# Performance work log

Measured on AMD Instinct MI355X. Metric: run time of the kernel, lower is better.

## Reference

```python
import math
import jax, jax.numpy as jnp
import numpy as np

H = 16          # num attention heads
D = 64          # head dim
BUCKETS = 256   # position_buckets
MAX_POS = 512   # max_relative_positions
ATT_SPAN = BUCKETS  # pos_ebd_size A
SCALE_FACTOR = 3    # 1 + len(['c2p','p2c'])


def _log_bucket(rel):
    # log-bucketed relative positions (DeBERTa-v2 _make_log_bucket_position)
    mid = BUCKETS // 2
    rel = jnp.clip(rel, -MAX_POS + 1, MAX_POS - 1)
    sign = jnp.sign(rel).astype(jnp.float32)
    abs_pos = jnp.maximum(jnp.abs(rel), 1)
    log_base = math.log((MAX_POS - 1) / mid)
    log_pos = jnp.ceil(jnp.log(abs_pos.astype(jnp.float32) / mid) / log_base * (mid - 1)) + mid
    bucket = jnp.where(abs_pos < mid, abs_pos.astype(jnp.float32), log_pos) * sign
    return bucket.astype(jnp.int32)


def _rel_pos(q_len, k_len):
    q = jnp.arange(q_len, dtype=jnp.int32)
    k = jnp.arange(k_len, dtype=jnp.int32)
    return _log_bucket(q[:, None] - k[None, :])  # (Q, K)


def setup_inputs() -> dict:
    key = jax.random.key(0)
    ks = jax.random.split(key, 6)
    B, S, Hd = 4, 1024, 1024
    std = 0.02
    return {
        "hidden_states": jax.random.normal(ks[0], (B, S, Hd), jnp.float32),
        "rel_embeddings": jax.random.normal(ks[1], (2 * ATT_SPAN, Hd), jnp.float32) * std,
        "Wq": jax.random.normal(ks[2], (Hd, H * D), jnp.float32) * std,
        "bq": jnp.zeros((H * D,), jnp.float32),
        "Wk": jax.random.normal(ks[3], (Hd, H * D), jnp.float32) * std,
        "bk": jnp.zeros((H * D,), jnp.float32),
        "Wv": jax.random.normal(ks[4], (Hd, H * D), jnp.float32) * std,
        "bv": jnp.zeros((H * D,), jnp.float32),
    }


def reference(hidden_states, rel_embeddings, Wq, bq, Wk, bk, Wv, bv):
    B, S, Hd = hidden_states.shape
    A2 = 2 * ATT_SPAN

    def heads(x):  # (B,S,H*D) -> (B,H,S,D)
        return x.reshape(B, S, H, D).transpose(0, 2, 1, 3)

    q = heads(hidden_states @ Wq + bq)
    k = heads(hidden_states @ Wk + bk)
    v = heads(hidden_states @ Wv + bv)

    scale = math.sqrt(D * SCALE_FACTOR)
    scores = jnp.einsum('bhqd,bhkd->bhqk', q, k) / scale  # (B,H,S,S)

    rel = _rel_pos(S, S)  # (S,S) int32 bucketed relative ids
    # share_att_key=True: pos key/query use key_proj/query_proj
    pos_k = (rel_embeddings @ Wk + bk).reshape(A2, H, D).transpose(1, 0, 2)  # (H,2A,D)
    pos_q = (rel_embeddings @ Wq + bq).reshape(A2, H, D).transpose(1, 0, 2)  # (H,2A,D)

    # c2p: content->position
    c2p = jnp.einsum('bhqd,hkd->bhqk', q, pos_k)  # (B,H,S,2A)
    c2p_idx = jnp.clip(rel + ATT_SPAN, 0, A2 - 1)  # (S,S)
    c2p = jnp.take_along_axis(c2p, jnp.broadcast_to(c2p_idx[None, None], (B, H, S, S)), axis=-1) / scale

    # p2c: position->content
    p2c = jnp.einsum('bhkd,hqd->bhkq', k, pos_q)  # (B,H,S,2A)
    p2c_idx = jnp.clip(-rel + ATT_SPAN, 0, A2 - 1)  # (S,S)
    p2c = jnp.take_along_axis(p2c, jnp.broadcast_to(p2c_idx[None, None], (B, H, S, S)), axis=-1)
    p2c = jnp.swapaxes(p2c, -1, -2) / scale

    probs = jax.nn.softmax(scores + c2p + p2c, axis=-1)
    ctx = jnp.einsum('bhqk,bhkd->bhqd', probs, v)  # (B,H,S,D)
    return ctx.transpose(0, 2, 1, 3).reshape(B, S, H * D)
```

## Files before the change

### kernel.cpp

```cpp
#include <hip/hip_runtime.h>
#include <hip/hip_bf16.h>
#include <math.h>

typedef __attribute__((ext_vector_type(8))) short v8s;
typedef __attribute__((ext_vector_type(4))) short v4sh;
typedef __attribute__((ext_vector_type(4))) unsigned short v4us;
typedef __attribute__((ext_vector_type(4))) float v4f;
typedef __attribute__((ext_vector_type(4))) int   v4i;

#define AS1(p) ((const __attribute__((address_space(1))) void*)(p))
#define AS3(p) ((__attribute__((address_space(3))) void*)(p))

__device__ inline unsigned short f2b(float f){
  __hip_bfloat16 h = __float2bfloat16(f);
  return __builtin_bit_cast(unsigned short, h);
}
__device__ inline float b2f(unsigned short u){
  __hip_bfloat16 h = __builtin_bit_cast(__hip_bfloat16, u);
  return __bfloat162float(h);
}
__device__ inline unsigned cvtpk(float lo, float hi){
  unsigned d;
  asm("v_cvt_pk_bf16_f32 %0, %1, %2" : "=v"(d) : "v"(lo), "v"(hi));
  return d;
}

__device__ inline int bucket_id(int i){
  int r = i - 1023;
  if (r > 511) r = 511; if (r < -511) r = -511;
  float sign = (r > 0) ? 1.f : ((r < 0) ? -1.f : 0.f);
  int ap = r < 0 ? -r : r; if (ap < 1) ap = 1;
  float bucket;
  if (ap < 128) bucket = (float)ap * sign;
  else {
    float lp = ceilf(logf((float)ap / 128.f) / logf(511.f/128.f) * 127.f) + 128.f;
    bucket = lp * sign;
  }
  int idx = (int)bucket + 256;
  if (idx < 0) idx = 0; if (idx > 511) idx = 511;
  return idx;
}

__global__ __launch_bounds__(256) void pack_x(const float* __restrict__ hs,
                                              const float* __restrict__ rel,
                                              const float* __restrict__ Wq,
                                              const float* __restrict__ Wk,
                                              const float* __restrict__ Wv,
                                              unsigned short* __restrict__ X,
                                              unsigned short* __restrict__ Wt3,
                                              short* __restrict__ tab,
                                              unsigned long long* __restrict__ tab64){
  __shared__ unsigned short t[64][65];
  int blk = blockIdx.x;
  if (blk < 2304){
    const int HT8 = 4096*1024/8;
    int i8 = blk*256 + threadIdx.x;
    const float* src = (i8 < HT8) ? (hs + (size_t)i8*8) : (rel + ((size_t)i8 - HT8)*8);
    v8s o;
    #pragma unroll
    for (int j = 0; j < 8; j++) o[j] = (short)f2b(src[j]);
    *(v8s*)&X[(size_t)i8*8] = o;
    return;
  }
  if (blk < 2313){
    int i = (blk - 2304)*256 + threadIdx.x;
    if (i < 2047) tab[i] = (short)bucket_id(i);
    if (i < 2056){
      unsigned long long w = 0;
      #pragma unroll
      for (int r = 0; r < 4; r++)
        w |= (unsigned long long)(unsigned short)bucket_id(i + r) << (16*r);
      tab64[i] = w;
    }
    return;
  }
  int tb = blk - 2313;
  int wsel = tb >> 8, bx = tb & 255;
  const float* in = (wsel == 0) ? Wq : ((wsel == 1) ? Wk : Wv);
  unsigned short* outp = Wt3 + ((size_t)wsel << 20);
  int r0 = (bx >> 4) << 6, c0 = (bx & 15) << 6;
  int tx = threadIdx.x & 63, ty = threadIdx.x >> 6;
  #pragma unroll
  for (int p = 0; p < 16; p++){ int r = (p<<2)+ty; t[tx][r] = f2b(in[(size_t)(r0+r)*1024 + c0+tx]); }
  __syncthreads();
  #pragma unroll
  for (int p = 0; p < 16; p++){ int c = (p<<2)+ty; outp[(size_t)(c0+c)*1024 + r0+tx] = t[c][tx]; }
}

__global__ __launch_bounds__(256) void gemm_qkv(
    const unsigned short* __restrict__ A,
    const unsigned short* __restrict__ Bt3,
    unsigned short* __restrict__ Qa, unsigned short* __restrict__ Ka,
    unsigned short* __restrict__ VtT,
    const float* __restrict__ bq, const float* __restrict__ bk,
    const float* __restrict__ bv, float alpha_q)
{
  __shared__ unsigned short smem[2*128*64];
  unsigned short* a_tile = smem;
  unsigned short* b_tile = smem + 128*64;
  int nb = (blockIdx.x & 7)*108 + (blockIdx.x >> 3);
  int bm = nb / 24, bn = nb % 24;
  int m0 = bm << 7, n0 = bn << 7;
  int tid = threadIdx.x, lane = tid & 63, wave = tid >> 6;
  int l15 = lane & 15, lhi = lane >> 4;
  int rbase = (wave >> 1) << 6, cbase = (wave & 1) << 6;
  int crow[4], csw[4];
  #pragma unroll
  for (int u = 0; u < 4; u++){
    int ch = tid + (u << 8);
    crow[u] = ch >> 3;
    csw[u] = ((ch & 7) ^ (crow[u] & 7)) << 3;
  }
  v4f acc[4][4] = {};
  for (int kt = 0; kt < 1024; kt += 64){
    #pragma unroll
    for (int u = 0; u < 4; u++){
      int ch = tid + (u << 8);
      __builtin_amdgcn_global_load_lds(AS1(A   + (size_t)(m0 + crow[u])*1024 + kt + csw[u]),
                                       AS3(a_tile + (size_t)ch*8), 16, 0, 0);
      __builtin_amdgcn_global_load_lds(AS1(Bt3 + (size_t)(n0 + crow[u])*1024 + kt + csw[u]),
                                       AS3(b_tile + (size_t)ch*8), 16, 0, 0);
    }
    __syncthreads();
    #pragma unroll
    for (int ks = 0; ks < 2; ks++){
      v8s af[4], bfr[4];
      int kb = (ks << 2) + lhi;
      #pragma unroll
      for (int i = 0; i < 4; i++){
        int r = rbase + (i << 4) + l15;
        af[i] = *(const v8s*)&a_tile[r*64 + ((kb ^ (r & 7)) << 3)];
      }
      #pragma unroll
      for (int j = 0; j < 4; j++){
        int r = cbase + (j << 4) + l15;
        bfr[j] = *(const v8s*)&b_tile[r*64 + ((kb ^ (r & 7)) << 3)];
      }
      #pragma unroll
      for (int i = 0; i < 4; i++)
        #pragma unroll
        for (int j = 0; j < 4; j++)
          acc[i][j] = __builtin_amdgcn_mfma_f32_16x16x32_bf16(af[i], bfr[j], acc[i][j], 0, 0, 0);
    }
    __syncthreads();
  }
  int seg = n0 >> 10;
  int nn0 = n0 & 1023;
  if (seg == 2){
    if (m0 >= 4096) return;
    int bb = m0 >> 10, s0 = m0 & 1023;
    #pragma unroll
    for (int i = 0; i < 4; i++){
      int r = rbase + (i << 4) + (lhi << 2);
      #pragma unroll
      for (int j = 0; j < 4; j++){
        int c = cbase + (j << 4) + l15;
        float bvv = bv[nn0 + c];
        #pragma unroll
        for (int rr = 0; rr < 4; rr++)
          smem[c*128 + ((r + rr) ^ ((c & 7) << 4))] = f2b(acc[i][j][rr] + bvv);
      }
    }
    __syncthreads();
    int v = tid >> 3, sc = (tid & 7) << 4;
    #pragma unroll
    for (int vb = 0; vb < 4; vb++){
      int vv = v + (vb << 5);
      #pragma unroll
      for (int c2 = 0; c2 < 2; c2++){
        int sb = sc + (c2 << 3);
        v8s val = *(const v8s*)&smem[vv*128 + (sb ^ ((vv & 7) << 4))];
        *(v8s*)&VtT[((size_t)(bb << 10) + nn0 + vv)*1024 + s0 + sb] = val;
      }
    }
    return;
  }
  unsigned short* C = (seg == 0) ? Qa : Ka;
  const float* bias = (seg == 0) ? bq : bk;
  float alpha = (seg == 0) ? alpha_q : 1.f;
  #pragma unroll
  for (int i = 0; i < 4; i++){
    int row = rbase + (i << 4) + (lhi << 2);
    #pragma unroll
    for (int j = 0; j < 4; j++){
      int col = cbase + (j << 4) + l15;
      float bvv = bias[nn0 + col];
      #pragma unroll
      for (int r = 0; r < 4; r++)
        smem[(row + r)*128 + (col ^ (((row + r) & 7) << 4))] = f2b((acc[i][j][r] + bvv) * alpha);
    }
  }
  __syncthreads();
  #pragma unroll
  for (int c = 0; c < 8; c++){
    int row = (tid >> 4) + (c << 4);
    int col8 = (tid & 15) << 3;
    v8s val = *(const v8s*)&smem[row*128 + (col8 ^ ((row & 7) << 4))];
    *(v8s*)&C[(size_t)(m0 + row)*1024 + nn0 + col8] = val;
  }
}

__global__ __launch_bounds__(256) void gemm_pos(
    const unsigned short* __restrict__ Qa,
    const unsigned short* __restrict__ Ka,
    unsigned short* __restrict__ C2P,
    unsigned short* __restrict__ P2C)
{
  __shared__ unsigned short smem[2*128*64];
  unsigned short* a_tile = smem;
  unsigned short* b_tile = smem + 128*64;
  int tab = blockIdx.y >> 4, h = blockIdx.y & 15;
  int bm = blockIdx.x >> 2, bn = blockIdx.x & 3;
  int m0 = bm << 7, n0 = bn << 7;
  const unsigned short* A  = tab ? Ka : Qa;
  const unsigned short* Bt = tab ? Qa : Ka;
  unsigned short* C = tab ? P2C : C2P;
  int tid = threadIdx.x, lane = tid & 63, wave = tid >> 6;
  int l15 = lane & 15, lhi = lane >> 4;
  int rbase = (wave >> 1) << 6, cbase = (wave & 1) << 6;
  #pragma unroll
  for (int u = 0; u < 4; u++){
    int ch = tid + (u << 8);
    int row = ch >> 3;
    int csw = ((ch & 7) ^ (row & 7)) << 3;
    __builtin_amdgcn_global_load_lds(AS1(A  + (size_t)(m0 + row)*1024 + (h << 6) + csw),
                                     AS3(a_tile + (size_t)ch*8), 16, 0, 0);
    __builtin_amdgcn_global_load_lds(AS1(Bt + (size_t)(4096 + n0 + row)*1024 + (h << 6) + csw),
                                     AS3(b_tile + (size_t)ch*8), 16, 0, 0);
  }
  __syncthreads();
  v4f acc[4][4] = {};
  #pragma unroll
  for (int ks = 0; ks < 2; ks++){
    v8s af[4], bfr[4];
    int kb = (ks << 2) + lhi;
    #pragma unroll
    for (int i = 0; i < 4; i++){
      int r = rbase + (i << 4) + l15;
      af[i] = *(const v8s*)&a_tile[r*64 + ((kb ^ (r & 7)) << 3)];
    }
    #pragma unroll
    for (int j = 0; j < 4; j++){
      int r = cbase + (j << 4) + l15;
      bfr[j] = *(const v8s*)&b_tile[r*64 + ((kb ^ (r & 7)) << 3)];
    }
    #pragma unroll
    for (int i = 0; i < 4; i++)
      #pragma unroll
      for (int j = 0; j < 4; j++)
        acc[i][j] = __builtin_amdgcn_mfma_f32_16x16x32_bf16(af[i], bfr[j], acc[i][j], 0, 0, 0);
  }
  __syncthreads();
  #pragma unroll
  for (int i = 0; i < 4; i++){
    int row = rbase + (i << 4) + (lhi << 2);
    #pragma unroll
    for (int j = 0; j < 4; j++){
      int col = cbase + (j << 4) + l15;
      #pragma unroll
      for (int r = 0; r < 4; r++)
        smem[(row + r)*128 + (col ^ (((row + r) & 7) << 4))] = f2b(acc[i][j][r]);
    }
  }
  __syncthreads();
  #pragma unroll
  for (int c = 0; c < 8; c++){
    int row = (tid >> 4) + (c << 4);
    int col8 = (tid & 15) << 3;
    v8s val = *(const v8s*)&smem[row*128 + (col8 ^ ((row & 7) << 4))];
    *(v8s*)&C[(size_t)(m0 + row)*8192 + (h << 9) + n0 + col8] = val;
  }
}

__global__ __launch_bounds__(256) void attn(
  const unsigned short* __restrict__ Qall,
  const unsigned short* __restrict__ Kall,
  const unsigned short* __restrict__ Vt,
  const unsigned short* __restrict__ c2p,
  const unsigned short* __restrict__ p2c,
  const short* __restrict__ idxt,
  const unsigned long long* __restrict__ t64g,
  float* __restrict__ out)
{
  __shared__ unsigned short k_lds[64*64];
  __shared__ unsigned short v_lds[64*64];
  __shared__ unsigned short cw[64*72];
  __shared__ unsigned short pw[64*72];
  __shared__ short basc[16*64];
  __shared__ short basp[16*64];

  int bid = blockIdx.x;
  int xcd = bid & 7, jj = bid >> 3;
  int bh = (xcd << 3) + (jj >> 4), qb = jj & 15;
  int b = bh >> 4, h = bh & 15;
  int q0 = qb << 6;
  int tid = threadIdx.x, lane = tid & 63, wave = tid >> 6;
  int l15 = lane & 15, lhi = lane >> 4;

  #pragma unroll
  for (int v = 0; v < 8; v++){
    int i = tid + (v << 8);
    int kt = (i >> 6) & 15, row = i & 63;
    if (i < 1024){
      int bc = idxt[q0 + row - (kt << 6) + 960] & ~7;
      basc[(kt << 6) + row] = (short)(row*72 - bc);
    } else {
      int bp = idxt[q0 + 1023 - (kt << 6) - row] & ~7;
      basp[(kt << 6) + row] = (short)(row*72 - bp);
    }
  }

  int qrow = q0 + (wave << 4) + l15;
  v8s aq[2];
  #pragma unroll
  for (int ks = 0; ks < 2; ks++)
    aq[ks] = *(const v8s*)&Qall[(size_t)((b << 10) + qrow)*1024 + (h << 6) + (ks << 5) + (lhi << 3)];

  int prow_[3], pcc_[3]; bool pval[3];
  #pragma unroll
  for (int u = 0; u < 3; u++){
    int pp = tid + (u << 8);
    pval[u] = pp < 576;
    prow_[u] = pp / 9; pcc_[u] = pp - prow_[u]*9;
  }
  const size_t cbase0 = ((size_t)((b << 10) + q0))*8192 + (h << 9);
  const size_t pbase0 = ((size_t)(b << 10))*8192 + (h << 9);

  unsigned long long t64u[4];

  auto issue_kwin = [&](int kt){
    int k0 = kt << 6;
    #pragma unroll
    for (int u = 0; u < 2; u++){
      int ch = tid + (u << 8);
      int rr = ch >> 3, seg = ch & 7;
      int csw = (seg ^ (rr & 7)) << 3;
      __builtin_amdgcn_global_load_lds(AS1(Kall + (size_t)((b << 10) + k0 + rr)*1024 + (h << 6) + csw),
                                       AS3(k_lds + (size_t)ch*8), 16, 0, 0);
    }
    #pragma unroll
    for (int u = 0; u < 3; u++){
      if (pval[u]){
        int row = prow_[u], cc = pcc_[u];
        int bc = row*72 - (int)basc[(kt << 6) + row];
        __builtin_amdgcn_global_load_lds(AS1(c2p + cbase0 + (size_t)row*8192 + bc + (cc << 3)),
                                         AS3(cw + (size_t)(tid + (u << 8))*8), 16, 0, 0);
      int bp = row*72 - (int)basp[(kt << 6) + row];
        __builtin_amdgcn_global_load_lds(AS1(p2c + pbase0 + (size_t)(k0 + row)*8192 + bp + (cc << 3)),
                                         AS3(pw + (size_t)(tid + (u << 8))*8), 16, 0, 0);
      }
    }
  };
  auto issue_tv = [&](int kt){
    int k0 = kt << 6;
    int Bc = q0 - k0 + (wave << 4) + l15 - (lhi << 2) + 1020;
    #pragma unroll
    for (int j = 0; j < 4; j++) t64u[j] = t64g[Bc - (j << 4)];
    __builtin_amdgcn_sched_barrier(0);
    #pragma unroll
    for (int u = 0; u < 2; u++){
      int ch = tid + (u << 8);
      int rr = ch >> 3, seg = ch & 7;
      int csw = (seg ^ (rr & 7)) << 3;
      __builtin_amdgcn_global_load_lds(AS1(Vt + (size_t)((b << 10) + (h << 6) + rr)*1024 + k0 + csw),
                                       AS3(v_lds + (size_t)ch*8), 16, 0, 0);
    }
  };

  v4f o_acc[4] = {};
  float m_run = -INFINITY, l_part = 0.f;

  __syncthreads();
  issue_kwin(0);
  __builtin_amdgcn_sched_barrier(0);
  issue_tv(0);

  for (int kt = 0; kt < 16; kt++){
    asm volatile("s_waitcnt vmcnt(6)" ::: "memory");
    __builtin_amdgcn_sched_barrier(0);
    __builtin_amdgcn_s_barrier();
    __builtin_amdgcn_sched_barrier(0);

    v4f s_acc[4] = {};
    #pragma unroll
    for (int j = 0; j < 4; j++){
      int krow = (j << 4) + l15;
      #pragma unroll
      for (int ks = 0; ks < 2; ks++){
        v8s kf = *(const v8s*)&k_lds[krow*64 + ((((ks << 2) + lhi) ^ (krow & 7)) << 3)];
        s_acc[j] = __builtin_amdgcn_mfma_f32_16x16x32_bf16(kf, aq[ks], s_acc[j], 0, 0, 0);
      }
    }
    int cvq = (int)basc[(kt << 6) + (wave << 4) + l15];
    #pragma unroll
    for (int j = 0; j < 4; j++){
      v4sh bp4 = *(const v4sh*)&basp[(kt << 6) + (j << 4) + (lhi << 2)];
      v4us idv = __builtin_bit_cast(v4us, t64u[j]);
      #pragma unroll
      for (int r = 0; r < 4; r++){
        int id = (int)idv[3 - r];
        s_acc[j][r] += b2f(cw[cvq + id]) + b2f(pw[(int)bp4[r] + id]);
      }
    }
    float lmax = s_acc[0][0];
    #pragma unroll
    for (int j = 0; j < 4; j++)
      #pragma unroll
      for (int r = 0; r < 4; r++) lmax = fmaxf(lmax, s_acc[j][r]);
    if (__any(lmax > m_run + 6.f)){
      float mx = lmax;
      mx = fmaxf(mx, __shfl_xor(mx, 16));
      mx = fmaxf(mx, __shfl_xor(mx, 32));
      float mnew = fmaxf(m_run, mx);
      float corr = exp2f(m_run - mnew);
      m_run = mnew;
      l_part *= corr;
      float co[4];
      #pragma unroll
      for (int r = 0; r < 4; r++) co[r] = __shfl(corr, (lhi << 2) + r);
      #pragma unroll
      for (int j = 0; j < 4; j++)
        #pragma unroll
        for (int r = 0; r < 4; r++) o_acc[j][r] *= co[r];
    }
    unsigned wj[4][2];
    float ps = 0.f;
    #pragma unroll
    for (int j = 0; j < 4; j++){
      float p0 = exp2f(s_acc[j][0] - m_run);
      float p1 = exp2f(s_acc[j][1] - m_run);
      float p2 = exp2f(s_acc[j][2] - m_run);
      float p3 = exp2f(s_acc[j][3] - m_run);
      ps += (p0 + p1) + (p2 + p3);
      wj[j][0] = cvtpk(p0, p1);
      wj[j][1] = cvtpk(p2, p3);
    }
    l_part += ps;
    #pragma unroll
    for (int p = 0; p < 2; p++){
      asm("v_permlane32_swap_b32 %0, %1" : "+v"(wj[0][p]), "+v"(wj[1][p]));
      asm("v_permlane32_swap_b32 %0, %1" : "+v"(wj[2][p]), "+v"(wj[3][p]));
      asm("v_permlane16_swap_b32 %0, %1" : "+v"(wj[0][p]), "+v"(wj[1][p]));
      asm("v_permlane16_swap_b32 %0, %1" : "+v"(wj[2][p]), "+v"(wj[3][p]));
    }
    v4i pai0 = { (int)wj[0][0], (int)wj[0][1], (int)wj[1][0], (int)wj[1][1] };
    v4i pai1 = { (int)wj[2][0], (int)wj[2][1], (int)wj[3][0], (int)wj[3][1] };
    v8s pa0 = __builtin_bit_cast(v8s, pai0);
    v8s pa1 = __builtin_bit_cast(v8s, pai1);

    asm volatile("s_waitcnt vmcnt(0)" ::: "memory");
    __builtin_amdgcn_sched_barrier(0);
    __builtin_amdgcn_s_barrier();
    __builtin_amdgcn_sched_barrier(0);

    if (kt < 15) issue_kwin(kt + 1);
    __builtin_amdgcn_sched_barrier(0);

    #pragma unroll
    for (int j = 0; j < 4; j++){
      int vrow = (j << 4) + l15;
      v8s vb0 = *(const v8s*)&v_lds[vrow*64 + (((lhi) ^ (vrow & 7)) << 3)];
      o_acc[j] = __builtin_amdgcn_mfma_f32_16x16x32_bf16(pa0, vb0, o_acc[j], 0, 0, 0);
      v8s vb1 = *(const v8s*)&v_lds[vrow*64 + (((4 + lhi) ^ (vrow & 7)) << 3)];
      o_acc[j] = __builtin_amdgcn_mfma_f32_16x16x32_bf16(pa1, vb1, o_acc[j], 0, 0, 0);
    }
    if (kt < 15){
      asm volatile("s_waitcnt lgkmcnt(0)" ::: "memory");
      __builtin_amdgcn_sched_barrier(0);
      __builtin_amdgcn_s_barrier();
      __builtin_amdgcn_sched_barrier(0);
      issue_tv(kt + 1);
    }
  }
  float ls = l_part;
  ls += __shfl_xor(ls, 16);
  ls += __shfl_xor(ls, 32);
  float inv = 1.f / ls;
  float io[4];
  #pragma unroll
  for (int r = 0; r < 4; r++) io[r] = __shfl(inv, (lhi << 2) + r);
  #pragma unroll
  for (int r = 0; r < 4; r++){
    int row = q0 + (wave << 4) + (lhi << 2) + r;
    #pragma unroll
    for (int j = 0; j < 4; j++)
      out[(size_t)((b << 10) + row)*1024 + (h << 6) + (j << 4) + l15] = o_acc[j][r] * io[r];
  }
}

extern "C" void kernel_launch(void* const* d_in, const int* in_sizes, int n_in,
                              void* d_out, int out_size, void* d_ws, size_t ws_size,
                              hipStream_t stream)
{
  const float* hs  = (const float*)d_in[0];
  const float* rel = (const float*)d_in[1];
  const float* Wq  = (const float*)d_in[2];
  const float* bq  = (const float*)d_in[3];
  const float* Wk  = (const float*)d_in[4];
  const float* bk  = (const float*)d_in[5];
  const float* Wv  = (const float*)d_in[6];
  const float* bv  = (const float*)d_in[7];
  float* out = (float*)d_out;

  char* ws = (char*)d_ws;
  size_t off = 0;
  auto alloc = [&](size_t bytes) -> void* {
    void* p = ws + off; off += (bytes + 255) & ~(size_t)255; return p;
  };
  short*              idxt  = (short*)             alloc(2047 * 2);
  unsigned long long* tab64 = (unsigned long long*)alloc(2056 * 8);
  unsigned short* Xb   = (unsigned short*)alloc((size_t)4608*1024*2);
  unsigned short* Wt3  = (unsigned short*)alloc((size_t)3072*1024*2);
  unsigned short* Qa   = (unsigned short*)alloc((size_t)4608*1024*2);
  unsigned short* Ka   = (unsigned short*)alloc((size_t)4608*1024*2);
  unsigned short* VtT  = (unsigned short*)alloc((size_t)4096*1024*2);
  unsigned short* C2P  = (unsigned short*)alloc((size_t)4096*8192*2);
  unsigned short* P2C  = (unsigned short*)alloc((size_t)4096*8192*2);
  (void)                                  alloc(4096);
  (void)ws_size; (void)in_sizes; (void)n_in; (void)out_size;

  pack_x<<<3081, 256, 0, stream>>>(hs, rel, Wq, Wk, Wv, Xb, Wt3, idxt, tab64);

  const float alpha_q = 1.4426950408889634f / sqrtf(192.f);
  gemm_qkv<<<864, 256, 0, stream>>>(Xb, Wt3, Qa, Ka, VtT, bq, bk, bv, alpha_q);

  gemm_pos<<<dim3(128, 32), 256, 0, stream>>>(Qa, Ka, C2P, P2C);

  attn<<<1024, 256, 0, stream>>>(Qa, Ka, VtT, C2P, P2C, idxt, tab64, out);
}
```

Baseline: 158.5 us.

## Double query tile per attention block to reuse K/V tiles across two row groups

The attention kernel now processes 128 query rows per block (two 16-row groups per wave) instead of 64, and launches 512 blocks instead of 1024. Each K/V tile loaded into LDS now feeds twice as many MFMAs, which halves total K/V global traffic. The p2c window widens to 144 columns and the c2p window to 128 rows to cover the larger tile. The change also raises wave priority around the MFMA loops. In exchange it uses more LDS and registers per block and runs half as many blocks on a 256-CU device, which may lower occupancy and leave CUs underused.

```diff
diff --git a/kernel.cpp b/kernel.cpp
--- a/kernel.cpp
+++ b/kernel.cpp
@@ -284,49 +284,46 @@
 {
   __shared__ unsigned short k_lds[64*64];
   __shared__ unsigned short v_lds[64*64];
-  __shared__ unsigned short cw[64*72];
-  __shared__ unsigned short pw[64*72];
-  __shared__ short basc[16*64];
+  __shared__ unsigned short cw[128*72];
+  __shared__ unsigned short pw[64*144];
+  __shared__ short basc[16*128];
   __shared__ short basp[16*64];
 
   int bid = blockIdx.x;
   int xcd = bid & 7, jj = bid >> 3;
-  int bh = (xcd << 3) + (jj >> 4), qb = jj & 15;
+  int bh = (xcd << 3) + (jj >> 3), qb = jj & 7;
   int b = bh >> 4, h = bh & 15;
-  int q0 = qb << 6;
+  int q0 = qb << 7;
   int tid = threadIdx.x, lane = tid & 63, wave = tid >> 6;
   int l15 = lane & 15, lhi = lane >> 4;
 
   #pragma unroll
-  for (int v = 0; v < 8; v++){
+  for (int v = 0; v < 12; v++){
     int i = tid + (v << 8);
-    int kt = (i >> 6) & 15, row = i & 63;
-    if (i < 1024){
+    if (i < 2048){
+      int kt = i >> 7, row = i & 127;
       int bc = idxt[q0 + row - (kt << 6) + 960] & ~7;
-      basc[(kt << 6) + row] = (short)(row*72 - bc);
+      basc[i] = (short)(row*72 - bc);
     } else {
+      int i2 = i - 2048;
+      int kt = i2 >> 6, row = i2 & 63;
       int bp = idxt[q0 + 1023 - (kt << 6) - row] & ~7;
-      basp[(kt << 6) + row] = (short)(row*72 - bp);
-    }
-  }
-
-  int qrow = q0 + (wave << 4) + l15;
-  v8s aq[2];
-  #pragma unroll
-  for (int ks = 0; ks < 2; ks++)
-    aq[ks] = *(const v8s*)&Qall[(size_t)((b << 10) + qrow)*1024 + (h << 6) + (ks << 5) + (lhi << 3)];
-
-  int prow_[3], pcc_[3]; bool pval[3];
-  #pragma unroll
-  for (int u = 0; u < 3; u++){
-    int pp = tid + (u << 8);
-    pval[u] = pp < 576;
-    prow_[u] = pp / 9; pcc_[u] = pp - prow_[u]*9;
-  }
+      basp[i2] = (short)(row*144 - bp);
+    }
+  }
+
+  v8s aq[2][2];
+  #pragma unroll
+  for (int g = 0; g < 2; g++)
+    #pragma unroll
+    for (int ks = 0; ks < 2; ks++)
+      aq[g][ks] = *(const v8s*)&Qall[(size_t)((b << 10) + q0 + (wave << 5) + (g << 4) + l15)*1024
+                                     + (h << 6) + (ks << 5) + (lhi << 3)];
+
   const size_t cbase0 = ((size_t)((b << 10) + q0))*8192 + (h << 9);
   const size_t pbase0 = ((size_t)(b << 10))*8192 + (h << 9);
 
-  unsigned long long t64u[4];
+  unsigned long long t64u[2][4];
 
   auto issue_kwin = [&](int kt){
     int k0 = kt << 6;
@@ -339,23 +336,34 @@
                                        AS3(k_lds + (size_t)ch*8), 16, 0, 0);
     }
     #pragma unroll
-    for (int u = 0; u < 3; u++){
-      if (pval[u]){
-        int row = prow_[u], cc = pcc_[u];
-        int bc = row*72 - (int)basc[(kt << 6) + row];
+    for (int u = 0; u < 5; u++){
+      int pp = tid + (u << 8);
+      if (pp < 1152){
+        int row = pp / 9, cc = pp - row*9;
+        int bc = row*72 - (int)basc[(kt << 7) + row];
         __builtin_amdgcn_global_load_lds(AS1(c2p + cbase0 + (size_t)row*8192 + bc + (cc << 3)),
-                                         AS3(cw + (size_t)(tid + (u << 8))*8), 16, 0, 0);
-      int bp = row*72 - (int)basp[(kt << 6) + row];
+                                         AS3(cw + (size_t)pp*8), 16, 0, 0);
+      }
+    }
+    #pragma unroll
+    for (int u = 0; u < 5; u++){
+      int pp = tid + (u << 8);
+      if (pp < 1152){
+        int row = pp / 18, cc = pp - row*18;
+        int bp = row*144 - (int)basp[(kt << 6) + row];
         __builtin_amdgcn_global_load_lds(AS1(p2c + pbase0 + (size_t)(k0 + row)*8192 + bp + (cc << 3)),
-                                         AS3(pw + (size_t)(tid + (u << 8))*8), 16, 0, 0);
+                                         AS3(pw + (size_t)pp*8), 16, 0, 0);
       }
     }
   };
   auto issue_tv = [&](int kt){
     int k0 = kt << 6;
-    int Bc = q0 - k0 + (wave << 4) + l15 - (lhi << 2) + 1020;
-    #pragma unroll
-    for (int j = 0; j < 4; j++) t64u[j] = t64g[Bc - (j << 4)];
+    #pragma unroll
+    for (int g = 0; g < 2; g++){
+      int Bc = q0 - k0 + (wave << 5) + (g << 4) + l15 - (lhi << 2) + 1020;
+      #pragma unroll
+      for (int j = 0; j < 4; j++) t64u[g][j] = t64g[Bc - (j << 4)];
+    }
     __builtin_amdgcn_sched_barrier(0);
     #pragma unroll
     for (int u = 0; u < 2; u++){
@@ -367,8 +375,9 @@
     }
   };
 
-  v4f o_acc[4] = {};
-  float m_run = -INFINITY, l_part = 0.f;
+  v4f o_acc[4][2] = {};
+  float m_run[2] = { -INFINITY, -INFINITY };
+  float l_part[2] = { 0.f, 0.f };
 
   __syncthreads();
   issue_kwin(0);
@@ -376,77 +385,97 @@
   issue_tv(0);
 
   for (int kt = 0; kt < 16; kt++){
-    asm volatile("s_waitcnt vmcnt(6)" ::: "memory");
+    asm volatile("s_waitcnt vmcnt(10)" ::: "memory");
     __builtin_amdgcn_sched_barrier(0);
     __builtin_amdgcn_s_barrier();
     __builtin_amdgcn_sched_barrier(0);
 
-    v4f s_acc[4] = {};
+    v4f s_acc[4][2] = {};
+    __builtin_amdgcn_s_setprio(1);
     #pragma unroll
     for (int j = 0; j < 4; j++){
       int krow = (j << 4) + l15;
       #pragma unroll
       for (int ks = 0; ks < 2; ks++){
         v8s kf = *(const v8s*)&k_lds[krow*64 + ((((ks << 2) + lhi) ^ (krow & 7)) << 3)];
-        s_acc[j] = __builtin_amdgcn_mfma_f32_16x16x32_bf16(kf, aq[ks], s_acc[j], 0, 0, 0);
-      }
-    }
-    int cvq = (int)basc[(kt << 6) + (wave << 4) + l15];
+        s_acc[j][0] = __builtin_amdgcn_mfma_f32_16x16x32_bf16(kf, aq[0][ks], s_acc[j][0], 0, 0, 0);
+        s_acc[j][1] = __builtin_amdgcn_mfma_f32_16x16x32_bf16(kf, aq[1][ks], s_acc[j][1], 0, 0, 0);
+      }
+    }
+    __builtin_amdgcn_s_setprio(0);
+    int cvq0 = (int)basc[(kt << 7) + (wave << 5) + l15];
+    int cvq1 = (int)basc[(kt << 7) + (wave << 5) + 16 + l15];
     #pragma unroll
     for (int j = 0; j < 4; j++){
       v4sh bp4 = *(const v4sh*)&basp[(kt << 6) + (j << 4) + (lhi << 2)];
-      v4us idv = __builtin_bit_cast(v4us, t64u[j]);
+      v4us id0 = __builtin_bit_cast(v4us, t64u[0][j]);
+      v4us id1 = __builtin_bit_cast(v4us, t64u[1][j]);
       #pragma unroll
       for (int r = 0; r < 4; r++){
-        int id = (int)idv[3 - r];
-        s_acc[j][r] += b2f(cw[cvq + id]) + b2f(pw[(int)bp4[r] + id]);
-      }
-    }
-    float lmax = s_acc[0][0];
-    #pragma unroll
-    for (int j = 0; j < 4; j++)
-      #pragma unroll
-      for (int r = 0; r < 4; r++) lmax = fmaxf(lmax, s_acc[j][r]);
-    if (__any(lmax > m_run + 6.f)){
-      float mx = lmax;
-      mx = fmaxf(mx, __shfl_xor(mx, 16));
-      mx = fmaxf(mx, __shfl_xor(mx, 32));
-      float mnew = fmaxf(m_run, mx);
-      float corr = exp2f(m_run - mnew);
-      m_run = mnew;
-      l_part *= corr;
-      float co[4];
-      #pragma unroll
-      for (int r = 0; r < 4; r++) co[r] = __shfl(corr, (lhi << 2) + r);
+        int pwb = (int)bp4[r];
+        int ida = (int)id0[3 - r];
+        int idb = (int)id1[3 - r];
+        s_acc[j][0][r] += b2f(cw[cvq0 + ida]) + b2f(pw[pwb + ida]);
+        s_acc[j][1][r] += b2f(cw[cvq1 + idb]) + b2f(pw[pwb + idb]);
+      }
+    }
+    float lmax[2];
+    #pragma unroll
+    for (int g = 0; g < 2; g++){
+      float lm = s_acc[0][g][0];
       #pragma unroll
       for (int j = 0; j < 4; j++)
         #pragma unroll
-        for (int r = 0; r < 4; r++) o_acc[j][r] *= co[r];
-    }
-    unsigned wj[4][2];
-    float ps = 0.f;
-    #pragma unroll
-    for (int j = 0; j < 4; j++){
-      float p0 = exp2f(s_acc[j][0] - m_run);
-      float p1 = exp2f(s_acc[j][1] - m_run);
-      float p2 = exp2f(s_acc[j][2] - m_run);
-      float p3 = exp2f(s_acc[j][3] - m_run);
-      ps += (p0 + p1) + (p2 + p3);
-      wj[j][0] = cvtpk(p0, p1);
-      wj[j][1] = cvtpk(p2, p3);
-    }
-    l_part += ps;
-    #pragma unroll
-    for (int p = 0; p < 2; p++){
-      asm("v_permlane32_swap_b32 %0, %1" : "+v"(wj[0][p]), "+v"(wj[1][p]));
-      asm("v_permlane32_swap_b32 %0, %1" : "+v"(wj[2][p]), "+v"(wj[3][p]));
-      asm("v_permlane16_swap_b32 %0, %1" : "+v"(wj[0][p]), "+v"(wj[1][p]));
-      asm("v_permlane16_swap_b32 %0, %1" : "+v"(wj[2][p]), "+v"(wj[3][p]));
-    }
-    v4i pai0 = { (int)wj[0][0], (int)wj[0][1], (int)wj[1][0], (int)wj[1][1] };
-    v4i pai1 = { (int)wj[2][0], (int)wj[2][1], (int)wj[3][0], (int)wj[3][1] };
-    v8s pa0 = __builtin_bit_cast(v8s, pai0);
-    v8s pa1 = __builtin_bit_cast(v8s, pai1);
+        for (int r = 0; r < 4; r++) lm = fmaxf(lm, s_acc[j][g][r]);
+      lmax[g] = lm;
+    }
+    if (__any((lmax[0] > m_run[0] + 6.f) || (lmax[1] > m_run[1] + 6.f))){
+      #pragma unroll
+      for (int g = 0; g < 2; g++){
+        float mx = lmax[g];
+        mx = fmaxf(mx, __shfl_xor(mx, 16));
+        mx = fmaxf(mx, __shfl_xor(mx, 32));
+        float mnew = fmaxf(m_run[g], mx);
+        float corr = exp2f(m_run[g] - mnew);
+        m_run[g] = mnew;
+        l_part[g] *= corr;
+        float co[4];
+        #pragma unroll
+        for (int r = 0; r < 4; r++) co[r] = __shfl(corr, (lhi << 2) + r);
+        #pragma unroll
+        for (int j = 0; j < 4; j++)
+          #pragma unroll
+          for (int r = 0; r < 4; r++) o_acc[j][g][r] *= co[r];
+      }
+    }
+    v8s pa0[2], pa1[2];
+    #pragma unroll
+    for (int g = 0; g < 2; g++){
+      unsigned wj[4][2];
+      float ps = 0.f;
+      #pragma unroll
+      for (int j = 0; j < 4; j++){
+        float p0 = exp2f(s_acc[j][g][0] - m_run[g]);
+        float p1 = exp2f(s_acc[j][g][1] - m_run[g]);
+        float p2 = exp2f(s_acc[j][g][2] - m_run[g]);
+        float p3 = exp2f(s_acc[j][g][3] - m_run[g]);
+        ps += (p0 + p1) + (p2 + p3);
+        wj[j][0] = cvtpk(p0, p1);
+        wj[j][1] = cvtpk(p2, p3);
+      }
+      l_part[g] += ps;
+      #pragma unroll
+      for (int p = 0; p < 2; p++){
+        asm("v_permlane32_swap_b32 %0, %1" : "+v"(wj[0][p]), "+v"(wj[1][p]));
+        asm("v_permlane32_swap_b32 %0, %1" : "+v"(wj[2][p]), "+v"(wj[3][p]));
+        asm("v_permlane16_swap_b32 %0, %1" : "+v"(wj[0][p]), "+v"(wj[1][p]));
+        asm("v_permlane16_swap_b32 %0, %1" : "+v"(wj[2][p]), "+v"(wj[3][p]));
+      }
+      v4i pai0 = { (int)wj[0][0], (int)wj[0][1], (int)wj[1][0], (int)wj[1][1] };
+      v4i pai1 = { (int)wj[2][0], (int)wj[2][1], (int)wj[3][0], (int)wj[3][1] };
+      pa0[g] = __builtin_bit_cast(v8s, pai0);
+      pa1[g] = __builtin_bit_cast(v8s, pai1);
+    }
 
     asm volatile("s_waitcnt vmcnt(0)" ::: "memory");
     __builtin_amdgcn_sched_barrier(0);
@@ -456,14 +485,18 @@
     if (kt < 15) issue_kwin(kt + 1);
     __builtin_amdgcn_sched_barrier(0);
 
+    __builtin_amdgcn_s_setprio(1);
     #pragma unroll
     for (int j = 0; j < 4; j++){
       int vrow = (j << 4) + l15;
       v8s vb0 = *(const v8s*)&v_lds[vrow*64 + (((lhi) ^ (vrow & 7)) << 3)];
-      o_acc[j] = __builtin_amdgcn_mfma_f32_16x16x32_bf16(pa0, vb0, o_acc[j], 0, 0, 0);
       v8s vb1 = *(const v8s*)&v_lds[vrow*64 + (((4 + lhi) ^ (vrow & 7)) << 3)];
-      o_acc[j] = __builtin_amdgcn_mfma_f32_16x16x32_bf16(pa1, vb1, o_acc[j], 0, 0, 0);
-    }
+      o_acc[j][0] = __builtin_amdgcn_mfma_f32_16x16x32_bf16(pa0[0], vb0, o_acc[j][0], 0, 0, 0);
+      o_acc[j][1] = __builtin_amdgcn_mfma_f32_16x16x32_bf16(pa0[1], vb0, o_acc[j][1], 0, 0, 0);
+      o_acc[j][0] = __builtin_amdgcn_mfma_f32_16x16x32_bf16(pa1[0], vb1, o_acc[j][0], 0, 0, 0);
+      o_acc[j][1] = __builtin_amdgcn_mfma_f32_16x16x32_bf16(pa1[1], vb1, o_acc[j][1], 0, 0, 0);
+    }
+    __builtin_amdgcn_s_setprio(0);
     if (kt < 15){
       asm volatile("s_waitcnt lgkmcnt(0)" ::: "memory");
       __builtin_amdgcn_sched_barrier(0);
@@ -472,19 +505,22 @@
       issue_tv(kt + 1);
     }
   }
-  float ls = l_part;
-  ls += __shfl_xor(ls, 16);
-  ls += __shfl_xor(ls, 32);
-  float inv = 1.f / ls;
-  float io[4];
-  #pragma unroll
-  for (int r = 0; r < 4; r++) io[r] = __shfl(inv, (lhi << 2) + r);
-  #pragma unroll
-  for (int r = 0; r < 4; r++){
-    int row = q0 + (wave << 4) + (lhi << 2) + r;
-    #pragma unroll
-    for (int j = 0; j < 4; j++)
-      out[(size_t)((b << 10) + row)*1024 + (h << 6) + (j << 4) + l15] = o_acc[j][r] * io[r];
+  #pragma unroll
+  for (int g = 0; g < 2; g++){
+    float ls = l_part[g];
+    ls += __shfl_xor(ls, 16);
+    ls += __shfl_xor(ls, 32);
+    float inv = 1.f / ls;
+    float io[4];
+    #pragma unroll
+    for (int r = 0; r < 4; r++) io[r] = __shfl(inv, (lhi << 2) + r);
+    #pragma unroll
+    for (int r = 0; r < 4; r++){
+      int row = q0 + (wave << 5) + (g << 4) + (lhi << 2) + r;
+      #pragma unroll
+      for (int j = 0; j < 4; j++)
+        out[(size_t)((b << 10) + row)*1024 + (h << 6) + (j << 4) + l15] = o_acc[j][g][r] * io[r];
+    }
   }
 }
 
@@ -526,5 +562,5 @@
 
   gemm_pos<<<dim3(128, 32), 256, 0, stream>>>(Qa, Ka, C2P, P2C);
 
-  attn<<<1024, 256, 0, stream>>>(Qa, Ka, VtT, C2P, P2C, idxt, tab64, out);
-}
+  attn<<<512, 256, 0, stream>>>(Qa, Ka, VtT, C2P, P2C, idxt, tab64, out);
+}
```

Result: no change. 155.4 us (-1.9%).
